# Kernel tuning notes

Hardware: AMD Instinct MI355X
Metric: run time of the kernel (lower is better)

Reference implementation:

```python
import jax, jax.numpy as jnp
import numpy as np

KD_T = 4.0
PATCH_NUM = 64
MASK_NUM = 8
BATCH = 256
DIM = 2048
P = PATCH_NUM - MASK_NUM  # 56


def setup_inputs() -> dict:
    key = jax.random.key(0)
    k1, k2, k3 = jax.random.split(key, 3)
    ebg = jax.random.normal(k1, (BATCH, DIM), dtype=jnp.float32)
    ebp = jax.random.normal(k2, (P * BATCH, DIM), dtype=jnp.float32)
    labels = jax.random.randint(k3, (BATCH,), 0, 10, dtype=jnp.int64)
    return {"ebg": ebg, "ebp": ebp, "labels": labels}


def _kl(y_s, y_t, T):
    # Faithful to KLDiv with dim=0 on vectors: softmax over the feature axis,
    # F.kl_div(..., reduction='batchmean') on a length-D vector divides by D.
    D = y_s.shape[-1]
    log_p_s = jax.nn.log_softmax(y_s / T, axis=-1)
    log_p_t = jax.nn.log_softmax(y_t / T, axis=-1)
    p_t = jnp.exp(log_p_t)
    return jnp.sum(p_t * (log_p_t - log_p_s), axis=-1) * (T * T / D)


def reference(ebg, ebp, labels):
    sg = jax.lax.stop_gradient
    ebp_r = ebp.reshape(P, BATCH, DIM)          # [P, B, D]
    ebp_bar = ebp_r.mean(axis=0)                # [B, D]

    # soft_dil_loss: sum over batch of symmetric KD with detached targets
    soft_dil = jnp.sum(_kl(ebg, sg(ebp_bar), KD_T)) + jnp.sum(_kl(ebp_bar, sg(ebg), KD_T))

    # soft_dcl_loss: per (batch, patch) pair on squared differences
    ebp_t = jnp.transpose(ebp_r, (1, 0, 2))     # [B, P, D]
    dg = (ebg[:, None, :] - ebp_t) ** 2         # [B, P, D]
    db = (ebp_bar[:, None, :] - ebp_t) ** 2     # [B, P, D]
    soft_dcl = (jnp.sum(_kl(dg, db, KD_T)) + jnp.sum(_kl(db, dg, KD_T))) / P

    return (soft_dil, soft_dcl)
```

## Files before the change

### kernel.cpp

```cpp
#include <hip/hip_runtime.h>
#include <math.h>

#define DIM   2048
#define BATCH 256
#define PN    56
constexpr float KD_T = 4.0f;

#define DCL_BLOCKS 896
#define DIL_BLOCKS 64

__device__ __forceinline__ float wave_sum(float v) {
#pragma unroll
    for (int o = 32; o > 0; o >>= 1) v += __shfl_xor(v, o, 64);
    return v;
}
__device__ __forceinline__ double wave_sum_d(double v) {
#pragma unroll
    for (int o = 32; o > 0; o >>= 1) v += __shfl_xor(v, o, 64);
    return v;
}

__global__ void __launch_bounds__(256) bar_kernel(const float* __restrict__ ebp,
                                                  float* __restrict__ bar) {
    int idx = blockIdx.x * 256 + threadIdx.x;
    const float4* ep = (const float4*)ebp;
    float x = 0.f, y = 0.f, z = 0.f, w = 0.f;
#pragma unroll 8
    for (int p = 0; p < PN; ++p) {
        float4 v = ep[(size_t)p * (BATCH * DIM / 4) + idx];
        x += v.x; y += v.y; z += v.z; w += v.w;
    }
    const float inv = 1.0f / PN;
    float4 o; o.x = x * inv; o.y = y * inv; o.z = z * inv; o.w = w * inv;
    ((float4*)bar)[idx] = o;
}

__global__ void __launch_bounds__(256) dil_kernel(const float* __restrict__ ebg,
                                                  const float* __restrict__ bar,
                                                  double* __restrict__ partial) {
    __shared__ double sd[4];
    const int lane = threadIdx.x & 63;
    const int wv   = threadIdx.x >> 6;
    const int row  = blockIdx.x * 4 + wv;
    const float4* g4 = (const float4*)(ebg + (size_t)row * DIM);
    const float4* m4 = (const float4*)(bar + (size_t)row * DIM);
    const float invT = 1.0f / KD_T;

    float ssum = 0.f, tsum = 0.f, t1 = 0.f, t2 = 0.f;
#pragma unroll
    for (int j = 0; j < 8; ++j) {
        float4 g = g4[j * 64 + lane];
        float4 m = m4[j * 64 + lane];
        float gs[4] = {g.x, g.y, g.z, g.w};
        float ms[4] = {m.x, m.y, m.z, m.w};
#pragma unroll
        for (int k = 0; k < 4; ++k) {
            float s = gs[k] * invT, t = ms[k] * invT;
            float es = __expf(s), et = __expf(t);
            float d = t - s;
            ssum += es; tsum += et;
            t1 = fmaf(es, d, t1);
            t2 = fmaf(et, d, t2);
        }
    }
    ssum = wave_sum(ssum); tsum = wave_sum(tsum);
    t1 = wave_sum(t1);     t2 = wave_sum(t2);
    double r = (double)(t2 / tsum - t1 / ssum);
    if (lane == 0) sd[wv] = r;
    __syncthreads();
    if (threadIdx.x == 0)
        partial[blockIdx.x] = (sd[0] + sd[1] + sd[2] + sd[3]) *
                              ((double)KD_T * KD_T / (double)DIM);
}

__global__ void __launch_bounds__(256) dcl_kernel(const float* __restrict__ ebg,
                                                  const float* __restrict__ ebp,
                                                  const float* __restrict__ bar,
                                                  double* __restrict__ partial) {
    __shared__ double sd[4];
    const int lane  = threadIdx.x & 63;
    const int wv    = threadIdx.x >> 6;
    const int gwave = blockIdx.x * 4 + wv;
    const int nwav  = DCL_BLOCKS * 4;
    const float invT = 1.0f / KD_T;

    double dacc = 0.0;
    for (int row = gwave; row < BATCH * PN; row += nwav) {
        const int b = row & (BATCH - 1);
        const float4* g4 = (const float4*)(ebg + (size_t)b * DIM);
        const float4* m4 = (const float4*)(bar + (size_t)b * DIM);
        const float4* e4 = (const float4*)(ebp + (size_t)row * DIM);

        float asum = 0.f, csum = 0.f, t1 = 0.f, t2 = 0.f;
#pragma unroll
        for (int j = 0; j < 8; ++j) {
            float4 g = g4[j * 64 + lane];
            float4 m = m4[j * 64 + lane];
            float4 e = e4[j * 64 + lane];
            float gs[4] = {g.x, g.y, g.z, g.w};
            float ms[4] = {m.x, m.y, m.z, m.w};
            float es[4] = {e.x, e.y, e.z, e.w};
#pragma unroll
            for (int k = 0; k < 4; ++k) {
                float dg = gs[k] - es[k];
                float db = ms[k] - es[k];
                float a = dg * dg * invT;
                float c = db * db * invT;
                float ea = __expf(a), ec = __expf(c);
                float d = c - a;
                asum += ea; csum += ec;
                t1 = fmaf(ea, d, t1);
                t2 = fmaf(ec, d, t2);
            }
        }
        asum = wave_sum(asum); csum = wave_sum(csum);
        t1 = wave_sum(t1);     t2 = wave_sum(t2);
        dacc += (double)(t2 / csum - t1 / asum);
    }
    if (lane == 0) sd[wv] = dacc;
    __syncthreads();
    if (threadIdx.x == 0)
        partial[blockIdx.x] = (sd[0] + sd[1] + sd[2] + sd[3]) *
                              ((double)KD_T * KD_T / (double)DIM / (double)PN);
}

__global__ void __launch_bounds__(256) finalize_kernel(const double* __restrict__ pdcl,
                                                       const double* __restrict__ pdil,
                                                       float* __restrict__ out) {
    __shared__ double sdc[4], sdl[4];
    const int t = threadIdx.x, lane = t & 63, wv = t >> 6;
    double vd = 0.0, vl = 0.0;
    for (int i = t; i < DCL_BLOCKS; i += 256) vd += pdcl[i];
    for (int i = t; i < DIL_BLOCKS; i += 256) vl += pdil[i];
    vd = wave_sum_d(vd); vl = wave_sum_d(vl);
    if (lane == 0) { sdc[wv] = vd; sdl[wv] = vl; }
    __syncthreads();
    if (t == 0) {
        out[0] = (float)(sdl[0] + sdl[1] + sdl[2] + sdl[3]);
        out[1] = (float)(sdc[0] + sdc[1] + sdc[2] + sdc[3]);
    }
}

extern "C" void kernel_launch(void* const* d_in, const int* in_sizes, int n_in,
                              void* d_out, int out_size, void* d_ws, size_t ws_size,
                              hipStream_t stream) {
    const float* ebg = (const float*)d_in[0];
    const float* ebp = (const float*)d_in[1];

    double* pdcl = (double*)d_ws;
    double* pdil = pdcl + DCL_BLOCKS;
    float*  bar  = (float*)((char*)d_ws + 8192);

    bar_kernel<<<BATCH * DIM / 4 / 256, 256, 0, stream>>>(ebp, bar);
    dil_kernel<<<DIL_BLOCKS, 256, 0, stream>>>(ebg, bar, pdil);
    dcl_kernel<<<DCL_BLOCKS, 256, 0, stream>>>(ebg, ebp, bar, pdcl);
    finalize_kernel<<<1, 256, 0, stream>>>(pdcl, pdil, (float*)d_out);
}
```

Before: 202.9 us.

## Fuse mean, DIL and DCL into one kernel staging ebp chunks in LDS

Merges the bar, dil and dcl kernels into a single kernel. Each block owns one batch row and half of the feature dimension, loads all 56 patch vectors for a 256-wide chunk into shared memory, computes the patch mean on the fly, and then evaluates the KL partial sums from the cached data. Previously ebp was read from HBM twice (once for the mean, once for DCL); now it is read once, and the two intermediate launches disappear. In exchange the block uses about 57 KB of LDS and 56 register accumulators per thread, which may limit occupancy. The softmax partial sums are now split across two blocks per row and combined in the finalize kernel.

```diff
diff --git a/kernel.cpp b/kernel.cpp
--- a/kernel.cpp
+++ b/kernel.cpp
@@ -1,13 +1,14 @@
 #include <hip/hip_runtime.h>
 #include <math.h>
 
-#define DIM   2048
-#define BATCH 256
-#define PN    56
+#define DIM    2048
+#define BATCH  256
+#define PN     56
+#define HALF   1024
+#define CHUNK  256
+#define NCHUNK 4
+#define NBLK   512
 constexpr float KD_T = 4.0f;
-
-#define DCL_BLOCKS 896
-#define DIL_BLOCKS 64
 
 __device__ __forceinline__ float wave_sum(float v) {
 #pragma unroll
@@ -20,124 +21,139 @@
     return v;
 }
 
-__global__ void __launch_bounds__(256) bar_kernel(const float* __restrict__ ebp,
-                                                  float* __restrict__ bar) {
-    int idx = blockIdx.x * 256 + threadIdx.x;
-    const float4* ep = (const float4*)ebp;
-    float x = 0.f, y = 0.f, z = 0.f, w = 0.f;
-#pragma unroll 8
-    for (int p = 0; p < PN; ++p) {
-        float4 v = ep[(size_t)p * (BATCH * DIM / 4) + idx];
-        x += v.x; y += v.y; z += v.z; w += v.w;
+__global__ void __launch_bounds__(256) fused_kernel(const float* __restrict__ ebg,
+                                                    const float* __restrict__ ebp,
+                                                    float* __restrict__ pdcl,
+                                                    float* __restrict__ pdil)
+{
+    __shared__ float ebp_s[PN * CHUNK];
+    __shared__ float bar_s[CHUNK];
+    __shared__ float redl[4][4];
+
+    const int t    = threadIdx.x;
+    const int lane = t & 63;
+    const int wv   = t >> 6;
+    const int bid  = blockIdx.x;
+    const int b    = bid >> 1;
+    const int half = bid & 1;
+    const float invT = 1.0f / KD_T;
+
+    float acc[14][4];
+#pragma unroll
+    for (int i = 0; i < 14; ++i)
+#pragma unroll
+        for (int j = 0; j < 4; ++j) acc[i][j] = 0.f;
+
+    float dss = 0.f, dts = 0.f, dt1 = 0.f, dt2 = 0.f;
+
+    const size_t browoff = (size_t)b * DIM + (size_t)half * HALF;
+
+    for (int c = 0; c < NCHUNK; ++c) {
+        const int base = c * CHUNK;
+
+        const float* ep = ebp + browoff + base + t;
+        float bsum = 0.f;
+#pragma unroll 14
+        for (int p = 0; p < PN; ++p) {
+            float v = ep[(size_t)p * (BATCH * DIM)];
+            bsum += v;
+            ebp_s[p * CHUNK + t] = v;
+        }
+        float barv = bsum * (1.0f / PN);
+        bar_s[t] = barv;
+        {
+            float g = ebg[browoff + base + t];
+            float s = g * invT, tv = barv * invT;
+            float es = __expf(s), et = __expf(tv);
+            float dd = tv - s;
+            dss += es; dts += et;
+            dt1 = fmaf(es, dd, dt1);
+            dt2 = fmaf(et, dd, dt2);
+        }
+        __syncthreads();
+
+        const float4 g4 = *(const float4*)(ebg + browoff + base + lane * 4);
+        const float4 m4 = *(const float4*)(bar_s + lane * 4);
+        const float gs[4] = {g4.x, g4.y, g4.z, g4.w};
+        const float ms[4] = {m4.x, m4.y, m4.z, m4.w};
+#pragma unroll
+        for (int i = 0; i < 14; ++i) {
+            const int p = wv * 14 + i;
+            float4 e = *(const float4*)(ebp_s + p * CHUNK + lane * 4);
+            float es_[4] = {e.x, e.y, e.z, e.w};
+#pragma unroll
+            for (int k = 0; k < 4; ++k) {
+                float dg = gs[k] - es_[k];
+                float db = ms[k] - es_[k];
+                float a  = dg * dg * invT;
+                float cc = db * db * invT;
+                float ea = __expf(a), ec = __expf(cc);
+                float d  = cc - a;
+                acc[i][0] += ea;
+                acc[i][1] += ec;
+                acc[i][2] = fmaf(ea, d, acc[i][2]);
+                acc[i][3] = fmaf(ec, d, acc[i][3]);
+            }
+        }
+        __syncthreads();
     }
-    const float inv = 1.0f / PN;
-    float4 o; o.x = x * inv; o.y = y * inv; o.z = z * inv; o.w = w * inv;
-    ((float4*)bar)[idx] = o;
+
+#pragma unroll
+    for (int i = 0; i < 14; ++i) {
+        float a0 = wave_sum(acc[i][0]);
+        float a1 = wave_sum(acc[i][1]);
+        float a2 = wave_sum(acc[i][2]);
+        float a3 = wave_sum(acc[i][3]);
+        if (lane == 0) {
+            float* q = pdcl + ((size_t)bid * PN + wv * 14 + i) * 4;
+            q[0] = a0; q[1] = a1; q[2] = a2; q[3] = a3;
+        }
+    }
+    dss = wave_sum(dss); dts = wave_sum(dts);
+    dt1 = wave_sum(dt1); dt2 = wave_sum(dt2);
+    if (lane == 0) { redl[wv][0] = dss; redl[wv][1] = dts; redl[wv][2] = dt1; redl[wv][3] = dt2; }
+    __syncthreads();
+    if (t == 0) {
+        float* q = pdil + (size_t)bid * 4;
+#pragma unroll
+        for (int j = 0; j < 4; ++j)
+            q[j] = redl[0][j] + redl[1][j] + redl[2][j] + redl[3][j];
+    }
 }
 
-__global__ void __launch_bounds__(256) dil_kernel(const float* __restrict__ ebg,
-                                                  const float* __restrict__ bar,
-                                                  double* __restrict__ partial) {
-    __shared__ double sd[4];
-    const int lane = threadIdx.x & 63;
-    const int wv   = threadIdx.x >> 6;
-    const int row  = blockIdx.x * 4 + wv;
-    const float4* g4 = (const float4*)(ebg + (size_t)row * DIM);
-    const float4* m4 = (const float4*)(bar + (size_t)row * DIM);
-    const float invT = 1.0f / KD_T;
-
-    float ssum = 0.f, tsum = 0.f, t1 = 0.f, t2 = 0.f;
-#pragma unroll
-    for (int j = 0; j < 8; ++j) {
-        float4 g = g4[j * 64 + lane];
-        float4 m = m4[j * 64 + lane];
-        float gs[4] = {g.x, g.y, g.z, g.w};
-        float ms[4] = {m.x, m.y, m.z, m.w};
-#pragma unroll
-        for (int k = 0; k < 4; ++k) {
-            float s = gs[k] * invT, t = ms[k] * invT;
-            float es = __expf(s), et = __expf(t);
-            float d = t - s;
-            ssum += es; tsum += et;
-            t1 = fmaf(es, d, t1);
-            t2 = fmaf(et, d, t2);
-        }
-    }
-    ssum = wave_sum(ssum); tsum = wave_sum(tsum);
-    t1 = wave_sum(t1);     t2 = wave_sum(t2);
-    double r = (double)(t2 / tsum - t1 / ssum);
-    if (lane == 0) sd[wv] = r;
-    __syncthreads();
-    if (threadIdx.x == 0)
-        partial[blockIdx.x] = (sd[0] + sd[1] + sd[2] + sd[3]) *
-                              ((double)KD_T * KD_T / (double)DIM);
-}
-
-__global__ void __launch_bounds__(256) dcl_kernel(const float* __restrict__ ebg,
-                                                  const float* __restrict__ ebp,
-                                                  const float* __restrict__ bar,
-                                                  double* __restrict__ partial) {
-    __shared__ double sd[4];
-    const int lane  = threadIdx.x & 63;
-    const int wv    = threadIdx.x >> 6;
-    const int gwave = blockIdx.x * 4 + wv;
-    const int nwav  = DCL_BLOCKS * 4;
-    const float invT = 1.0f / KD_T;
-
-    double dacc = 0.0;
-    for (int row = gwave; row < BATCH * PN; row += nwav) {
-        const int b = row & (BATCH - 1);
-        const float4* g4 = (const float4*)(ebg + (size_t)b * DIM);
-        const float4* m4 = (const float4*)(bar + (size_t)b * DIM);
-        const float4* e4 = (const float4*)(ebp + (size_t)row * DIM);
-
-        float asum = 0.f, csum = 0.f, t1 = 0.f, t2 = 0.f;
-#pragma unroll
-        for (int j = 0; j < 8; ++j) {
-            float4 g = g4[j * 64 + lane];
-            float4 m = m4[j * 64 + lane];
-            float4 e = e4[j * 64 + lane];
-            float gs[4] = {g.x, g.y, g.z, g.w};
-            float ms[4] = {m.x, m.y, m.z, m.w};
-            float es[4] = {e.x, e.y, e.z, e.w};
-#pragma unroll
-            for (int k = 0; k < 4; ++k) {
-                float dg = gs[k] - es[k];
-                float db = ms[k] - es[k];
-                float a = dg * dg * invT;
-                float c = db * db * invT;
-                float ea = __expf(a), ec = __expf(c);
-                float d = c - a;
-                asum += ea; csum += ec;
-                t1 = fmaf(ea, d, t1);
-                t2 = fmaf(ec, d, t2);
-            }
-        }
-        asum = wave_sum(asum); csum = wave_sum(csum);
-        t1 = wave_sum(t1);     t2 = wave_sum(t2);
-        dacc += (double)(t2 / csum - t1 / asum);
-    }
-    if (lane == 0) sd[wv] = dacc;
-    __syncthreads();
-    if (threadIdx.x == 0)
-        partial[blockIdx.x] = (sd[0] + sd[1] + sd[2] + sd[3]) *
-                              ((double)KD_T * KD_T / (double)DIM / (double)PN);
-}
-
-__global__ void __launch_bounds__(256) finalize_kernel(const double* __restrict__ pdcl,
-                                                       const double* __restrict__ pdil,
-                                                       float* __restrict__ out) {
+__global__ void __launch_bounds__(256) finalize_kernel(const float* __restrict__ pdcl,
+                                                       const float* __restrict__ pdil,
+                                                       float* __restrict__ out)
+{
     __shared__ double sdc[4], sdl[4];
     const int t = threadIdx.x, lane = t & 63, wv = t >> 6;
-    double vd = 0.0, vl = 0.0;
-    for (int i = t; i < DCL_BLOCKS; i += 256) vd += pdcl[i];
-    for (int i = t; i < DIL_BLOCKS; i += 256) vl += pdil[i];
-    vd = wave_sum_d(vd); vl = wave_sum_d(vl);
-    if (lane == 0) { sdc[wv] = vd; sdl[wv] = vl; }
+    const int b = t;
+
+    double dsum = 0.0;
+    for (int p = 0; p < PN; ++p) {
+        const float* q0 = pdcl + ((size_t)(b * 2 + 0) * PN + p) * 4;
+        const float* q1 = pdcl + ((size_t)(b * 2 + 1) * PN + p) * 4;
+        double asum = (double)q0[0] + q1[0];
+        double csum = (double)q0[1] + q1[1];
+        double t1   = (double)q0[2] + q1[2];
+        double t2   = (double)q0[3] + q1[3];
+        dsum += t2 / csum - t1 / asum;
+    }
+    const float* r0 = pdil + (size_t)(b * 2 + 0) * 4;
+    const float* r1 = pdil + (size_t)(b * 2 + 1) * 4;
+    double ss = (double)r0[0] + r1[0];
+    double ts = (double)r0[1] + r1[1];
+    double u1 = (double)r0[2] + r1[2];
+    double u2 = (double)r0[3] + r1[3];
+    double lsum = u2 / ts - u1 / ss;
+
+    dsum = wave_sum_d(dsum); lsum = wave_sum_d(lsum);
+    if (lane == 0) { sdc[wv] = dsum; sdl[wv] = lsum; }
     __syncthreads();
     if (t == 0) {
-        out[0] = (float)(sdl[0] + sdl[1] + sdl[2] + sdl[3]);
-        out[1] = (float)(sdc[0] + sdc[1] + sdc[2] + sdc[3]);
+        double kT2 = (double)KD_T * KD_T;
+        out[0] = (float)((sdl[0] + sdl[1] + sdl[2] + sdl[3]) * (kT2 / DIM));
+        out[1] = (float)((sdc[0] + sdc[1] + sdc[2] + sdc[3]) * (kT2 / DIM / PN));
     }
 }
 
@@ -147,12 +163,9 @@
     const float* ebg = (const float*)d_in[0];
     const float* ebp = (const float*)d_in[1];
 
-    double* pdcl = (double*)d_ws;
-    double* pdil = pdcl + DCL_BLOCKS;
-    float*  bar  = (float*)((char*)d_ws + 8192);
+    float* pdcl = (float*)d_ws;
+    float* pdil = pdcl + (size_t)NBLK * PN * 4;
 
-    bar_kernel<<<BATCH * DIM / 4 / 256, 256, 0, stream>>>(ebp, bar);
-    dil_kernel<<<DIL_BLOCKS, 256, 0, stream>>>(ebg, bar, pdil);
-    dcl_kernel<<<DCL_BLOCKS, 256, 0, stream>>>(ebg, ebp, bar, pdcl);
+    fused_kernel<<<NBLK, 256, 0, stream>>>(ebg, ebp, pdcl, pdil);
     finalize_kernel<<<1, 256, 0, stream>>>(pdcl, pdil, (float*)d_out);
 }
```

Result: no change. 204.4 us (+0.7%).

## Fuse mean and dil KL into one kernel and rebalance dcl grid

Applied to the files above, without the earlier changes.

The patch-mean computation and the dil KL term now run in one element-parallel kernel. Each block writes four per-block partial sums, and the finalize kernel combines them per row in double precision. This removes a separate low-occupancy dil launch and a re-read of the mean buffer. The dcl kernel drops its grid-stride loop in favour of twice as many blocks, each handling exactly two rows. The mean loads change from float4 to scalar loads, which could reduce per-thread memory-level parallelism.

```diff
diff --git a/kernel.cpp b/kernel.cpp
--- a/kernel.cpp
+++ b/kernel.cpp
@@ -1,13 +1,13 @@
 #include <hip/hip_runtime.h>
 #include <math.h>
 
-#define DIM   2048
-#define BATCH 256
-#define PN    56
+#define DIM    2048
+#define BATCH  256
+#define PN     56
+#define BDIM   (BATCH * DIM)
+#define ABLK   2048
+#define BBLK   1792
 constexpr float KD_T = 4.0f;
-
-#define DCL_BLOCKS 896
-#define DIL_BLOCKS 64
 
 __device__ __forceinline__ float wave_sum(float v) {
 #pragma unroll
@@ -20,94 +20,86 @@
     return v;
 }
 
-__global__ void __launch_bounds__(256) bar_kernel(const float* __restrict__ ebp,
-                                                  float* __restrict__ bar) {
-    int idx = blockIdx.x * 256 + threadIdx.x;
-    const float4* ep = (const float4*)ebp;
-    float x = 0.f, y = 0.f, z = 0.f, w = 0.f;
-#pragma unroll 8
-    for (int p = 0; p < PN; ++p) {
-        float4 v = ep[(size_t)p * (BATCH * DIM / 4) + idx];
-        x += v.x; y += v.y; z += v.z; w += v.w;
-    }
-    const float inv = 1.0f / PN;
-    float4 o; o.x = x * inv; o.y = y * inv; o.z = z * inv; o.w = w * inv;
-    ((float4*)bar)[idx] = o;
-}
-
-__global__ void __launch_bounds__(256) dil_kernel(const float* __restrict__ ebg,
-                                                  const float* __restrict__ bar,
-                                                  double* __restrict__ partial) {
-    __shared__ double sd[4];
-    const int lane = threadIdx.x & 63;
-    const int wv   = threadIdx.x >> 6;
-    const int row  = blockIdx.x * 4 + wv;
-    const float4* g4 = (const float4*)(ebg + (size_t)row * DIM);
-    const float4* m4 = (const float4*)(bar + (size_t)row * DIM);
+__global__ void __launch_bounds__(256) bar_dil_kernel(const float* __restrict__ ebg,
+                                                      const float* __restrict__ ebp,
+                                                      float* __restrict__ barw,
+                                                      float* __restrict__ pdil)
+{
+    __shared__ float red[4][4];
+    const int t    = threadIdx.x;
+    const int lane = t & 63;
+    const int wv   = t >> 6;
+    const int idx  = blockIdx.x * 256 + t;
     const float invT = 1.0f / KD_T;
 
-    float ssum = 0.f, tsum = 0.f, t1 = 0.f, t2 = 0.f;
+    const float* p0 = ebp + idx;
+    float a0 = 0.f, a1 = 0.f, a2 = 0.f, a3 = 0.f;
 #pragma unroll
-    for (int j = 0; j < 8; ++j) {
-        float4 g = g4[j * 64 + lane];
-        float4 m = m4[j * 64 + lane];
-        float gs[4] = {g.x, g.y, g.z, g.w};
-        float ms[4] = {m.x, m.y, m.z, m.w};
+    for (int p = 0; p < PN; p += 4) {
+        a0 += p0[(size_t)(p + 0) * BDIM];
+        a1 += p0[(size_t)(p + 1) * BDIM];
+        a2 += p0[(size_t)(p + 2) * BDIM];
+        a3 += p0[(size_t)(p + 3) * BDIM];
+    }
+    const float bar = (a0 + a1 + a2 + a3) * (1.0f / PN);
+    barw[idx] = bar;
+
+    const float g  = ebg[idx];
+    const float s  = g * invT, tv = bar * invT;
+    const float es = __expf(s), et = __expf(tv);
+    const float dd = tv - s;
+    float dss = es, dts = et, dt1 = es * dd, dt2 = et * dd;
+
+    dss = wave_sum(dss); dts = wave_sum(dts);
+    dt1 = wave_sum(dt1); dt2 = wave_sum(dt2);
+    if (lane == 0) { red[wv][0] = dss; red[wv][1] = dts; red[wv][2] = dt1; red[wv][3] = dt2; }
+    __syncthreads();
+    if (t == 0) {
+        float* qp = pdil + (size_t)blockIdx.x * 4;
 #pragma unroll
-        for (int k = 0; k < 4; ++k) {
-            float s = gs[k] * invT, t = ms[k] * invT;
-            float es = __expf(s), et = __expf(t);
-            float d = t - s;
-            ssum += es; tsum += et;
-            t1 = fmaf(es, d, t1);
-            t2 = fmaf(et, d, t2);
-        }
+        for (int k = 0; k < 4; ++k)
+            qp[k] = red[0][k] + red[1][k] + red[2][k] + red[3][k];
     }
-    ssum = wave_sum(ssum); tsum = wave_sum(tsum);
-    t1 = wave_sum(t1);     t2 = wave_sum(t2);
-    double r = (double)(t2 / tsum - t1 / ssum);
-    if (lane == 0) sd[wv] = r;
-    __syncthreads();
-    if (threadIdx.x == 0)
-        partial[blockIdx.x] = (sd[0] + sd[1] + sd[2] + sd[3]) *
-                              ((double)KD_T * KD_T / (double)DIM);
 }
 
 __global__ void __launch_bounds__(256) dcl_kernel(const float* __restrict__ ebg,
+                                                  const float* __restrict__ barw,
                                                   const float* __restrict__ ebp,
-                                                  const float* __restrict__ bar,
-                                                  double* __restrict__ partial) {
+                                                  double* __restrict__ pdcl)
+{
     __shared__ double sd[4];
-    const int lane  = threadIdx.x & 63;
-    const int wv    = threadIdx.x >> 6;
-    const int gwave = blockIdx.x * 4 + wv;
-    const int nwav  = DCL_BLOCKS * 4;
+    const int t    = threadIdx.x;
+    const int lane = t & 63;
+    const int wv   = t >> 6;
+    const int gw   = blockIdx.x * 4 + wv;
     const float invT = 1.0f / KD_T;
 
     double dacc = 0.0;
-    for (int row = gwave; row < BATCH * PN; row += nwav) {
-        const int b = row & (BATCH - 1);
-        const float4* g4 = (const float4*)(ebg + (size_t)b * DIM);
-        const float4* m4 = (const float4*)(bar + (size_t)b * DIM);
-        const float4* e4 = (const float4*)(ebp + (size_t)row * DIM);
+#pragma unroll
+    for (int rr = 0; rr < 2; ++rr) {
+        const int row = gw * 2 + rr;
+        const int b   = row & (BATCH - 1);
+        const float4* e4 = (const float4*)(ebp  + (size_t)row * DIM);
+        const float4* g4 = (const float4*)(ebg  + (size_t)b   * DIM);
+        const float4* m4 = (const float4*)(barw + (size_t)b   * DIM);
 
         float asum = 0.f, csum = 0.f, t1 = 0.f, t2 = 0.f;
 #pragma unroll
         for (int j = 0; j < 8; ++j) {
+            float4 e = e4[j * 64 + lane];
             float4 g = g4[j * 64 + lane];
             float4 m = m4[j * 64 + lane];
-            float4 e = e4[j * 64 + lane];
-            float gs[4] = {g.x, g.y, g.z, g.w};
-            float ms[4] = {m.x, m.y, m.z, m.w};
-            float es[4] = {e.x, e.y, e.z, e.w};
+            float es_[4] = {e.x, e.y, e.z, e.w};
+            float gs[4]  = {g.x, g.y, g.z, g.w};
+            float ms[4]  = {m.x, m.y, m.z, m.w};
 #pragma unroll
             for (int k = 0; k < 4; ++k) {
-                float dg = gs[k] - es[k];
-                float db = ms[k] - es[k];
-                float a = dg * dg * invT;
-                float c = db * db * invT;
-                float ea = __expf(a), ec = __expf(c);
-                float d = c - a;
+                float dg = gs[k] - es_[k];
+                float db = ms[k] - es_[k];
+                float a   = dg * dg * invT;
+                float cc2 = db * db * invT;
+                float ea = __expf(a), ec = __expf(cc2);
+                float d  = cc2 - a;
                 asum += ea; csum += ec;
                 t1 = fmaf(ea, d, t1);
                 t2 = fmaf(ec, d, t2);
@@ -119,25 +111,35 @@
     }
     if (lane == 0) sd[wv] = dacc;
     __syncthreads();
-    if (threadIdx.x == 0)
-        partial[blockIdx.x] = (sd[0] + sd[1] + sd[2] + sd[3]) *
-                              ((double)KD_T * KD_T / (double)DIM / (double)PN);
+    if (t == 0) pdcl[blockIdx.x] = sd[0] + sd[1] + sd[2] + sd[3];
 }
 
 __global__ void __launch_bounds__(256) finalize_kernel(const double* __restrict__ pdcl,
-                                                       const double* __restrict__ pdil,
-                                                       float* __restrict__ out) {
+                                                       const float* __restrict__ pdil,
+                                                       float* __restrict__ out)
+{
     __shared__ double sdc[4], sdl[4];
     const int t = threadIdx.x, lane = t & 63, wv = t >> 6;
-    double vd = 0.0, vl = 0.0;
-    for (int i = t; i < DCL_BLOCKS; i += 256) vd += pdcl[i];
-    for (int i = t; i < DIL_BLOCKS; i += 256) vl += pdil[i];
+
+    double vd = 0.0;
+    for (int i = t; i < BBLK; i += 256) vd += pdcl[i];
+
+    const float* base = pdil + (size_t)t * 8 * 4;
+    double ss = 0.0, ts = 0.0, u1 = 0.0, u2 = 0.0;
+#pragma unroll
+    for (int k = 0; k < 8; ++k) {
+        float4 v = *(const float4*)(base + k * 4);
+        ss += v.x; ts += v.y; u1 += v.z; u2 += v.w;
+    }
+    double vl = u2 / ts - u1 / ss;
+
     vd = wave_sum_d(vd); vl = wave_sum_d(vl);
     if (lane == 0) { sdc[wv] = vd; sdl[wv] = vl; }
     __syncthreads();
     if (t == 0) {
-        out[0] = (float)(sdl[0] + sdl[1] + sdl[2] + sdl[3]);
-        out[1] = (float)(sdc[0] + sdc[1] + sdc[2] + sdc[3]);
+        const double kT2 = (double)KD_T * KD_T;
+        out[0] = (float)((sdl[0] + sdl[1] + sdl[2] + sdl[3]) * (kT2 / DIM));
+        out[1] = (float)((sdc[0] + sdc[1] + sdc[2] + sdc[3]) * (kT2 / DIM / PN));
     }
 }
 
@@ -147,12 +149,11 @@
     const float* ebg = (const float*)d_in[0];
     const float* ebp = (const float*)d_in[1];
 
-    double* pdcl = (double*)d_ws;
-    double* pdil = pdcl + DCL_BLOCKS;
-    float*  bar  = (float*)((char*)d_ws + 8192);
+    float*  barw = (float*)d_ws;
+    float*  pdil = barw + (size_t)BATCH * DIM;
+    double* pdcl = (double*)(pdil + (size_t)ABLK * 4);
 
-    bar_kernel<<<BATCH * DIM / 4 / 256, 256, 0, stream>>>(ebp, bar);
-    dil_kernel<<<DIL_BLOCKS, 256, 0, stream>>>(ebg, bar, pdil);
-    dcl_kernel<<<DCL_BLOCKS, 256, 0, stream>>>(ebg, ebp, bar, pdcl);
+    bar_dil_kernel<<<ABLK, 256, 0, stream>>>(ebg, ebp, barw, pdil);
+    dcl_kernel<<<BBLK, 256, 0, stream>>>(ebg, barw, ebp, pdcl);
     finalize_kernel<<<1, 256, 0, stream>>>(pdcl, pdil, (float*)d_out);
 }
```

New measurement: 198.9 us. No clear change (-1.9%).
